# Optimization experiments

Measured on AMD Instinct MI355X. Metric: run time of the kernel, lower is better.

## Reference

```python
import jax, jax.numpy as jnp
import numpy as np

H = 512   # layer_size
D = 5     # dim
B = 64
T = 512
EPS = 1e-3  # Keras BatchNormalization default epsilon


def _p(key, shape, scale=0.05):
    return jax.random.normal(key, shape, dtype=jnp.float32) * scale


def setup_inputs() -> dict:
    key = jax.random.key(0)
    ks = jax.random.split(key, 32)
    inp = {
        "x": jax.random.normal(ks[0], (B, T, D), dtype=jnp.float32),
        # LSTM 1 (input D)
        "W1": _p(ks[1], (D, 4 * H)), "U1": _p(ks[2], (H, 4 * H)), "b1": jnp.zeros((4 * H,), jnp.float32),
        # BatchNorm on H features (inference: moving stats)
        "g1": jnp.ones((H,), jnp.float32), "be1": jnp.zeros((H,), jnp.float32),
        "m1": _p(ks[3], (H,), 0.1), "v1": jnp.ones((H,), jnp.float32) + jax.random.uniform(ks[4], (H,)) * 0.1,
        # LSTM 2 (input H)
        "W2": _p(ks[5], (H, 4 * H)), "U2": _p(ks[6], (H, 4 * H)), "b2": jnp.zeros((4 * H,), jnp.float32),
        # LSTM 3 (input H, returns last state only)
        "W3": _p(ks[7], (H, 4 * H)), "U3": _p(ks[8], (H, 4 * H)), "b3": jnp.zeros((4 * H,), jnp.float32),
        # dense head y
        "d1w": _p(ks[9], (H, 32)), "d1b": jnp.zeros((32,), jnp.float32),
        "g2": jnp.ones((32,), jnp.float32), "be2": jnp.zeros((32,), jnp.float32),
        "m2": _p(ks[10], (32,), 0.1), "v2": jnp.ones((32,), jnp.float32) + jax.random.uniform(ks[11], (32,)) * 0.1,
        "d2w": _p(ks[12], (32, 16)), "d2b": jnp.zeros((16,), jnp.float32),
        "hw": _p(ks[13], (16, 1)), "hb": jnp.zeros((1,), jnp.float32),
        # dense head z
        "d4w": _p(ks[14], (H, 128)), "d4b": jnp.zeros((128,), jnp.float32),
        "d5w": _p(ks[15], (128, 64)), "d5b": jnp.zeros((64,), jnp.float32),
        "rw": _p(ks[16], (64, D)), "rb": jnp.zeros((D,), jnp.float32),
    }
    return inp


def lstm(x, W, U, b):
    """Keras LSTM, gate order i,f,c,o. x: [B,T,din] -> (seq [B,T,H], h_T, c_T)."""
    xz = jnp.einsum('btd,dk->btk', x, W) + b  # precompute input projections [B,T,4H]

    def step(carry, xz_t):
        h, c = carry
        z = xz_t + h @ U
        i, f, g, o = jnp.split(z, 4, axis=-1)
        i = jax.nn.sigmoid(i)
        f = jax.nn.sigmoid(f)
        g = jnp.tanh(g)
        o = jax.nn.sigmoid(o)
        c = f * c + i * g
        h = o * jnp.tanh(c)
        return (h, c), h

    b_ = x.shape[0]
    h0 = jnp.zeros((b_, U.shape[0]), x.dtype)
    (hT, cT), hs = jax.lax.scan(step, (h0, h0), jnp.swapaxes(xz, 0, 1))
    return jnp.swapaxes(hs, 0, 1), hT, cT


def bn_inf(x, g, b, m, v):
    return (x - m) * (g / jnp.sqrt(v + EPS)) + b


def reference(x, W1, U1, b1, g1, be1, m1, v1, W2, U2, b2, W3, U3, b3,
              d1w, d1b, g2, be2, m2, v2, d2w, d2b, hw, hb,
              d4w, d4b, d5w, d5b, rw, rb):
    # inference: GaussianNoise / Dropout are identity
    x1, h1, s1 = lstm(x, W1, U1, b1)          # [B,T,H]
    xr = bn_inf(x1, g1, be1, m1, v1)
    x2, h2, s2 = lstm(xr, W2, U2, b2)         # [B,T,H]
    xs = x1 + x2                               # residual Add
    _, h3, s3 = lstm(xs, W3, U3, b3)           # last hidden state [B,H]
    xlast = h3
    # head y
    y = xlast @ d1w + d1b
    y = bn_inf(y, g2, be2, m2, v2)
    y = y @ d2w + d2b
    y = jax.nn.sigmoid(y @ hw + hb)            # [B,1]
    # head z
    z = xlast @ d4w + d4b
    z = z @ d5w + d5b
    z = z @ rw + rb                            # [B,D]
    return (y, z)
```

## Files before the change

### kernel.cpp

```cpp
#include <hip/hip_runtime.h>
#include <hip/hip_bf16.h>

typedef short bf16x8 __attribute__((ext_vector_type(8)));
typedef float f32x4 __attribute__((ext_vector_type(4)));
typedef unsigned short u16;
typedef unsigned int u32;
typedef unsigned long long u64;

#define EPSBN 1e-3f

__device__ __forceinline__ u16 f2b(float f){
  unsigned u = __float_as_uint(f);
  return (u16)((u + 0x7fffu + ((u >> 16) & 1u)) >> 16);
}
__device__ __forceinline__ float b2f(u16 v){ return __uint_as_float(((unsigned)v) << 16); }
__device__ __forceinline__ float sigm(float x){ return 1.f/(1.f + __expf(-x)); }
__device__ __forceinline__ float tanhx(float x){ return 2.f/(1.f + __expf(-2.f*x)) - 1.f; }

union U64x2 { u64 q[2]; bf16x8 v; };


__global__ void prep_sv(const float* __restrict__ g1, const float* __restrict__ be1,
                        const float* __restrict__ m1, const float* __restrict__ v1,
                        float* __restrict__ s, float* __restrict__ tv){
  int k = blockIdx.x*256 + threadIdx.x;
  if (k < 512){
    float sv = g1[k] * rsqrtf(v1[k] + EPSBN);
    s[k] = sv;
    tv[k] = be1[k] - m1[k]*sv;
  }
}

__global__ void prep_b2p(const float* __restrict__ W2, const float* __restrict__ b2,
                         const float* __restrict__ tv, float* __restrict__ out){
  int col = blockIdx.x*256 + threadIdx.x;
  float acc = b2[col];
  for (int k=0;k<512;++k) acc += tv[k] * W2[(size_t)k*2048 + col];
  out[col] = acc;
}

__global__ void transpose_pack(const float* __restrict__ in, const float* __restrict__ scale,
                               u16* __restrict__ out){
  __shared__ float tile[64][65];
  int k0 = blockIdx.x * 64;
  int c0 = blockIdx.y * 64;
  int t = threadIdx.x;
  int cc = t & 63, kk0 = (t >> 6) * 16;
  #pragma unroll
  for (int i=0;i<16;++i){
    float v = in[(size_t)(k0 + kk0 + i)*2048 + c0 + cc];
    if (scale) v *= scale[k0 + kk0 + i];
    tile[kk0 + i][cc] = v;
  }
  __syncthreads();
  int cc2 = t >> 2, kp = t & 3;
  int col = c0 + cc2;
  int hcol = col & 511;
  int row = (hcol >> 5)*128 + (col >> 9)*32 + ((hcol >> 4) & 1)*16 + (col & 15);
  bf16x8 v0, v1;
  #pragma unroll
  for (int i=0;i<8;++i){
    v0[i] = (short)f2b(tile[kp*16 + i][cc2]);
    v1[i] = (short)f2b(tile[kp*16 + 8 + i][cc2]);
  }
  u16* dst = out + (size_t)row*512 + k0 + kp*16;
  *(bf16x8*)dst = v0;
  *(bf16x8*)(dst + 8) = v1;
}

__global__ void pack_w1(const float* __restrict__ W1, u16* __restrict__ out){
  int r = blockIdx.x*256 + threadIdx.x;
  int wg = r >> 7, q = (r >> 5) & 3, jt = (r >> 4) & 1, jj = r & 15;
  int col = q*512 + wg*32 + jt*16 + jj;
  #pragma unroll
  for (int k=0;k<32;++k)
    out[(size_t)r*32 + k] = (k < 5) ? f2b(W1[(size_t)k*2048 + col]) : (u16)0;
}

__global__ void pack_x(const float* __restrict__ x, u16* __restrict__ out){
  int i = blockIdx.x*256 + threadIdx.x;
  int k = i & 31;
  int bt = i >> 5;
  out[i] = (k < 5) ? f2b(x[(size_t)bt*5 + k]) : (u16)0;
}

__device__ __forceinline__ void pollge(const u32* p, u32 target){
  while (__hip_atomic_load(p, __ATOMIC_RELAXED, __HIP_MEMORY_SCOPE_AGENT) < target) {}
}

__global__ void __launch_bounds__(512, 2) scan_all(
    const u16* __restrict__ Ure1, const u16* __restrict__ Ure2, const u16* __restrict__ Ure3,
    const u16* __restrict__ W1p,  const u16* __restrict__ W2p,  const u16* __restrict__ W3p,
    const u16* __restrict__ xpad,
    const float* __restrict__ b1, const float* __restrict__ b2p, const float* __restrict__ b3,
    u32* __restrict__ hbuf_all,
    u32* __restrict__ x1seq,
    u32* __restrict__ xsseq,
    float* __restrict__ h3out, u32* __restrict__ cnt)
{
  const int bid = blockIdx.x;
  const int phase = bid >> 6;
  const int b6 = bid & 63;
  const int g = b6 & 3, wg = b6 >> 2;
  const int tid = threadIdx.x;
  const int w = tid >> 6, l = tid & 63;
  const int lm = l & 15, lh = (l >> 4) & 3;
  const int kp = w & 3, jt = w >> 2;
  const int bg0 = g * 16;
  const int jp = tid & 15, gb = (tid >> 4) & 15;
  const int jt2 = jp >> 3;

  const u16* Ure  = phase == 0 ? Ure1 : (phase == 1 ? Ure2 : Ure3);
  const u16* Wre  = phase == 0 ? W1p  : (phase == 1 ? W2p  : W3p);
  const float* bias = phase == 0 ? b1 : (phase == 1 ? b2p : b3);
  u32* hbuf32 = hbuf_all + (size_t)phase * 32768;
  u32* seqout = phase == 0 ? x1seq : (phase == 1 ? xsseq : nullptr);
  const u32* upseq = phase == 1 ? x1seq : (phase == 2 ? xsseq : nullptr);

  u32* cq  = cnt + (phase*4 + g)*64;
  const u32* upq = (phase > 0) ? cnt + ((phase-1)*4 + g)*64 : nullptr;

  bf16x8 aU[4][4];
  #pragma unroll
  for (int q=0;q<4;++q){
    const u16* up = Ure + (size_t)(wg*128 + q*32 + jt*16 + lm)*512 + kp*128 + lh*8;
    #pragma unroll
    for (int ks=0;ks<4;++ks) aU[q][ks] = *(const bf16x8*)(up + ks*32);
  }
  bf16x8 aW[4][4];
  bf16x8 aW1[4];
  if (phase == 0){
    if (kp == 0){
      #pragma unroll
      for (int q=0;q<4;++q)
        aW1[q] = *(const bf16x8*)(Wre + (size_t)(wg*128 + q*32 + jt*16 + lm)*32 + lh*8);
    }
  } else {
    #pragma unroll
    for (int q=0;q<4;++q){
      const u16* wp = Wre + (size_t)(wg*128 + q*32 + jt*16 + lm)*512 + kp*128 + lh*8;
      #pragma unroll
      for (int ks=0;ks<4;++ks) aW[q][ks] = *(const bf16x8*)(wp + ks*32);
    }
  }

  float bias0[4], bias1[4];
  if (tid < 256){
    #pragma unroll
    for (int q=0;q<4;++q){
      bias0[q] = bias[q*512 + wg*32 + 2*jp];
      bias1[q] = bias[q*512 + wg*32 + 2*jp + 1];
    }
  }

  float cs0 = 0.f, cs1 = 0.f;

  __shared__ float zex[8][4][16][18];
  const u64* hbase = (const u64*)hbuf32;

  for (int t=0; t<512; ++t){
    f32x4 acc[4] = {};
    u32 rv = 0;

    if (phase == 0){
      if (kp == 0){
        bf16x8 bx = *(const bf16x8*)(xpad + ((size_t)(bg0+lm)*512 + t)*32 + lh*8);
        #pragma unroll
        for (int q=0;q<4;++q)
          acc[q] = __builtin_amdgcn_mfma_f32_16x16x32_bf16(aW1[q], bx, acc[q], 0,0,0);
      }
    } else {
      pollge(upq, (u32)(16*(t+1)));
      if (phase == 1 && tid < 256)
        rv = __hip_atomic_load(upseq + ((size_t)(bg0+gb)*512 + t)*256 + wg*16 + jp,
                               __ATOMIC_RELAXED, __HIP_MEMORY_SCOPE_AGENT);
      const u64* xp = (const u64*)upseq + ((size_t)(bg0+lm)*512 + t)*128 + kp*32 + lh*2;
      U64x2 xq[4];
      #pragma unroll
      for (int ks=0;ks<4;++ks){
        xq[ks].q[0] = __hip_atomic_load(xp + ks*8,     __ATOMIC_RELAXED, __HIP_MEMORY_SCOPE_AGENT);
        xq[ks].q[1] = __hip_atomic_load(xp + ks*8 + 1, __ATOMIC_RELAXED, __HIP_MEMORY_SCOPE_AGENT);
      }
      #pragma unroll
      for (int ks=0;ks<4;++ks){
        #pragma unroll
        for (int q=0;q<4;++q)
          acc[q] = __builtin_amdgcn_mfma_f32_16x16x32_bf16(aW[q][ks], xq[ks].v, acc[q], 0,0,0);
      }
    }

    pollge(cq, (u32)(16*t));
    {
      const u64* hp = hbase + (size_t)(((t+1)&1)*64 + bg0 + lm)*128 + kp*32 + lh*2;
      U64x2 hq[4];
      #pragma unroll
      for (int ks=0;ks<4;++ks){
        hq[ks].q[0] = __hip_atomic_load(hp + ks*8,     __ATOMIC_RELAXED, __HIP_MEMORY_SCOPE_AGENT);
        hq[ks].q[1] = __hip_atomic_load(hp + ks*8 + 1, __ATOMIC_RELAXED, __HIP_MEMORY_SCOPE_AGENT);
      }
      #pragma unroll
      for (int ks=0;ks<4;++ks){
        #pragma unroll
        for (int q=0;q<4;++q)
          acc[q] = __builtin_amdgcn_mfma_f32_16x16x32_bf16(aU[q][ks], hq[ks].v, acc[q], 0,0,0);
      }
    }

    #pragma unroll
    for (int q=0;q<4;++q){
      #pragma unroll
      for (int r=0;r<4;++r)
        zex[q*2+jt][kp][lh*4 + r][lm] = acc[q][r];
    }
    __syncthreads();

    if (tid < 256){
      const int r0 = (2*jp) & 15, r1 = r0 + 1;
      float zv0[4], zv1[4];
      #pragma unroll
      for (int q=0;q<4;++q){
        const int ti = q*2 + jt2;
        zv0[q] = zex[ti][0][r0][gb] + zex[ti][1][r0][gb]
               + zex[ti][2][r0][gb] + zex[ti][3][r0][gb] + bias0[q];
        zv1[q] = zex[ti][0][r1][gb] + zex[ti][1][r1][gb]
               + zex[ti][2][r1][gb] + zex[ti][3][r1][gb] + bias1[q];
      }
      float iv = sigm(zv0[0]), fv = sigm(zv0[1]), gv = tanhx(zv0[2]), ov = sigm(zv0[3]);
      cs0 = fv * cs0 + iv * gv;
      float hv0 = ov * tanhx(cs0);
      iv = sigm(zv1[0]); fv = sigm(zv1[1]); gv = tanhx(zv1[2]); ov = sigm(zv1[3]);
      cs1 = fv * cs1 + iv * gv;
      float hv1 = ov * tanhx(cs1);

      const u32 pw = (u32)f2b(hv0) | ((u32)f2b(hv1) << 16);
      __hip_atomic_store(hbuf32 + (size_t)((t&1)*64 + bg0 + gb)*256 + wg*16 + jp, pw,
                         __ATOMIC_RELAXED, __HIP_MEMORY_SCOPE_AGENT);
      if (phase == 0){
        __hip_atomic_store(seqout + ((size_t)(bg0+gb)*512 + t)*256 + wg*16 + jp, pw,
                           __ATOMIC_RELAXED, __HIP_MEMORY_SCOPE_AGENT);
      } else if (phase == 1){
        float x1r0 = b2f((u16)(rv & 0xffffu));
        float x1r1 = b2f((u16)(rv >> 16));
        u32 sv = (u32)f2b(x1r0 + hv0) | ((u32)f2b(x1r1 + hv1) << 16);
        __hip_atomic_store(seqout + ((size_t)(bg0+gb)*512 + t)*256 + wg*16 + jp, sv,
                           __ATOMIC_RELAXED, __HIP_MEMORY_SCOPE_AGENT);
      } else if (t == 511){
        h3out[(size_t)(bg0+gb)*512 + wg*32 + 2*jp]     = hv0;
        h3out[(size_t)(bg0+gb)*512 + wg*32 + 2*jp + 1] = hv1;
      }
    }
    __syncthreads();
    if (tid == 0)
      __hip_atomic_fetch_add(cq, 1u, __ATOMIC_RELAXED, __HIP_MEMORY_SCOPE_AGENT);
  }
}

__global__ void __launch_bounds__(256) head_k(
    const float* __restrict__ h3,
    const float* __restrict__ d1w, const float* __restrict__ d1b,
    const float* __restrict__ g2, const float* __restrict__ be2,
    const float* __restrict__ m2, const float* __restrict__ v2,
    const float* __restrict__ d2w, const float* __restrict__ d2b,
    const float* __restrict__ hw, const float* __restrict__ hb,
    const float* __restrict__ d4w, const float* __restrict__ d4b,
    const float* __restrict__ d5w, const float* __restrict__ d5b,
    const float* __restrict__ rw, const float* __restrict__ rb,
    float* __restrict__ out)
{
  __shared__ float hl[512];
  __shared__ float a1[32], a2[16], c1[128], c2[64];
  int b = blockIdx.x, t = threadIdx.x;
  for (int i=t; i<512; i+=256) hl[i] = h3[(size_t)b*512 + i];
  __syncthreads();
  if (t < 32){
    float acc = d1b[t];
    for (int k=0;k<512;++k) acc += hl[k] * d1w[(size_t)k*32 + t];
    a1[t] = (acc - m2[t]) * (g2[t] * rsqrtf(v2[t] + EPSBN)) + be2[t];
  } else if (t >= 128){
    int i = t - 128;
    float acc = d4b[i];
    for (int k=0;k<512;++k) acc += hl[k] * d4w[(size_t)k*128 + i];
    c1[i] = acc;
  }
  __syncthreads();
  if (t < 16){
    float acc = d2b[t];
    for (int k=0;k<32;++k) acc += a1[k] * d2w[k*16 + t];
    a2[t] = acc;
  } else if (t >= 64 && t < 128){
    int i = t - 64;
    float acc = d5b[i];
    for (int k=0;k<128;++k) acc += c1[k] * d5w[k*64 + i];
    c2[i] = acc;
  }
  __syncthreads();
  if (t == 0){
    float acc = hb[0];
    for (int k=0;k<16;++k) acc += a2[k] * hw[k];
    out[b] = 1.f/(1.f + __expf(-acc));
  } else if (t >= 32 && t < 37){
    int i = t - 32;
    float acc = rb[i];
    for (int k=0;k<64;++k) acc += c2[k] * rw[k*5 + i];
    out[64 + b*5 + i] = acc;
  }
}

extern "C" void kernel_launch(void* const* d_in, const int* in_sizes, int n_in,
                              void* d_out, int out_size, void* d_ws, size_t ws_size,
                              hipStream_t stream)
{
  const float* x   = (const float*)d_in[0];
  const float* W1  = (const float*)d_in[1];
  const float* U1  = (const float*)d_in[2];
  const float* b1  = (const float*)d_in[3];
  const float* g1  = (const float*)d_in[4];
  const float* be1 = (const float*)d_in[5];
  const float* m1  = (const float*)d_in[6];
  const float* v1  = (const float*)d_in[7];
  const float* W2  = (const float*)d_in[8];
  const float* U2  = (const float*)d_in[9];
  const float* b2  = (const float*)d_in[10];
  const float* W3  = (const float*)d_in[11];
  const float* U3  = (const float*)d_in[12];
  const float* b3  = (const float*)d_in[13];
  const float* d1w = (const float*)d_in[14];
  const float* d1b = (const float*)d_in[15];
  const float* g2  = (const float*)d_in[16];
  const float* be2 = (const float*)d_in[17];
  const float* m2  = (const float*)d_in[18];
  const float* v2  = (const float*)d_in[19];
  const float* d2w = (const float*)d_in[20];
  const float* d2b = (const float*)d_in[21];
  const float* hw  = (const float*)d_in[22];
  const float* hb  = (const float*)d_in[23];
  const float* d4w = (const float*)d_in[24];
  const float* d4b = (const float*)d_in[25];
  const float* d5w = (const float*)d_in[26];
  const float* d5b = (const float*)d_in[27];
  const float* rw  = (const float*)d_in[28];
  const float* rb  = (const float*)d_in[29];

  char* ws = (char*)d_ws;
  constexpr size_t SZ_W   = 2048ull*512*2;
  constexpr size_t o_Ure1 = 0;
  constexpr size_t o_Ure2 = o_Ure1 + SZ_W;
  constexpr size_t o_Ure3 = o_Ure2 + SZ_W;
  constexpr size_t o_W2p  = o_Ure3 + SZ_W;
  constexpr size_t o_W3p  = o_W2p + SZ_W;
  constexpr size_t o_W1p  = o_W3p + SZ_W;
  constexpr size_t o_xpad = o_W1p + 2048ull*32*2;
  constexpr size_t o_b2p  = o_xpad + 64ull*512*32*2;
  constexpr size_t o_s    = o_b2p + 2048ull*4;
  constexpr size_t o_tv   = o_s + 512ull*4;
  constexpr size_t o_h3   = o_tv + 512ull*4;
  constexpr size_t o_h    = o_h3 + 64ull*512*4;
  constexpr size_t SZ_HP  = 2ull*64*256*4;
  constexpr size_t SZ_H   = 3*SZ_HP;
  constexpr size_t o_cnt  = o_h + SZ_H;
  constexpr size_t o_x1   = o_cnt + 4096;
  constexpr size_t o_xs   = o_x1 + 64ull*512*512*2;

  u16* Ure1 = (u16*)(ws + o_Ure1);
  u16* Ure2 = (u16*)(ws + o_Ure2);
  u16* Ure3 = (u16*)(ws + o_Ure3);
  u16* W2p  = (u16*)(ws + o_W2p);
  u16* W3p  = (u16*)(ws + o_W3p);
  u16* W1p  = (u16*)(ws + o_W1p);
  u16* xpad = (u16*)(ws + o_xpad);
  u32* x1p  = (u32*)(ws + o_x1);
  u32* xsp  = (u32*)(ws + o_xs);

  hipMemsetAsync(ws + o_h, 0, SZ_H + 4096, stream);

  prep_sv<<<dim3(2), dim3(256), 0, stream>>>(g1, be1, m1, v1, (float*)(ws+o_s), (float*)(ws+o_tv));
  transpose_pack<<<dim3(8,32), dim3(256), 0, stream>>>(U1, nullptr, Ure1);
  transpose_pack<<<dim3(8,32), dim3(256), 0, stream>>>(U2, nullptr, Ure2);
  transpose_pack<<<dim3(8,32), dim3(256), 0, stream>>>(U3, nullptr, Ure3);
  transpose_pack<<<dim3(8,32), dim3(256), 0, stream>>>(W3, nullptr, W3p);
  transpose_pack<<<dim3(8,32), dim3(256), 0, stream>>>(W2, (const float*)(ws+o_s), W2p);
  prep_b2p<<<dim3(8), dim3(256), 0, stream>>>(W2, b2, (const float*)(ws+o_tv), (float*)(ws+o_b2p));
  pack_w1<<<dim3(8), dim3(256), 0, stream>>>(W1, W1p);
  pack_x<<<dim3(4096), dim3(256), 0, stream>>>(x, xpad);

  scan_all<<<dim3(192), dim3(512), 0, stream>>>(
      Ure1, Ure2, Ure3, W1p, W2p, W3p, xpad,
      b1, (const float*)(ws+o_b2p), b3,
      (u32*)(ws+o_h), x1p, xsp,
      (float*)(ws+o_h3), (u32*)(ws+o_cnt));

  head_k<<<dim3(64), dim3(256), 0, stream>>>((const float*)(ws+o_h3),
      d1w, d1b, g2, be2, m2, v2, d2w, d2b, hw, hb, d4w, d4b, d5w, d5b, rw, rb,
      (float*)d_out);
}
```

Measured before the change: 2.629 ms.

## Prefetch next-step input projection and signal per-wave completion before barrier

Moves the next timestep's input loads (x, or the upstream layer's sequence plus residual) so they are issued after the current recurrent state is fetched, overlapping them with the U-matrix MFMAs. Each of the four writing waves now drains its own stores and bumps the counter itself, so completion is signalled before the trailing block barrier rather than after it. Polling targets are scaled by four to match the per-wave increments. Empty asm constraints pin the weight fragments in registers. The cost is higher register pressure, and the per-wave vmcnt(0) wait plus relaxed ordering depend on the stores being visible before the counter increment.

```diff
diff --git a/kernel.cpp b/kernel.cpp
--- a/kernel.cpp
+++ b/kernel.cpp
@@ -93,9 +93,7 @@
     const u16* __restrict__ W1p,  const u16* __restrict__ W2p,  const u16* __restrict__ W3p,
     const u16* __restrict__ xpad,
     const float* __restrict__ b1, const float* __restrict__ b2p, const float* __restrict__ b3,
-    u32* __restrict__ hbuf_all,
-    u32* __restrict__ x1seq,
-    u32* __restrict__ xsseq,
+    u32* __restrict__ hbuf_all, u32* __restrict__ x1seq, u32* __restrict__ xsseq,
     float* __restrict__ h3out, u32* __restrict__ cnt)
 {
   const int bid = blockIdx.x;
@@ -125,22 +123,30 @@
   for (int q=0;q<4;++q){
     const u16* up = Ure + (size_t)(wg*128 + q*32 + jt*16 + lm)*512 + kp*128 + lh*8;
     #pragma unroll
-    for (int ks=0;ks<4;++ks) aU[q][ks] = *(const bf16x8*)(up + ks*32);
+    for (int ks=0;ks<4;++ks){
+      aU[q][ks] = *(const bf16x8*)(up + ks*32);
+      asm volatile("" : "+v"(aU[q][ks]));
+    }
   }
   bf16x8 aW[4][4];
   bf16x8 aW1[4];
   if (phase == 0){
     if (kp == 0){
       #pragma unroll
-      for (int q=0;q<4;++q)
+      for (int q=0;q<4;++q){
         aW1[q] = *(const bf16x8*)(Wre + (size_t)(wg*128 + q*32 + jt*16 + lm)*32 + lh*8);
+        asm volatile("" : "+v"(aW1[q]));
+      }
     }
   } else {
     #pragma unroll
     for (int q=0;q<4;++q){
       const u16* wp = Wre + (size_t)(wg*128 + q*32 + jt*16 + lm)*512 + kp*128 + lh*8;
       #pragma unroll
-      for (int ks=0;ks<4;++ks) aW[q][ks] = *(const bf16x8*)(wp + ks*32);
+      for (int ks=0;ks<4;++ks){
+        aW[q][ks] = *(const bf16x8*)(wp + ks*32);
+        asm volatile("" : "+v"(aW[q][ks]));
+      }
     }
   }
 
@@ -158,29 +164,36 @@
   __shared__ float zex[8][4][16][18];
   const u64* hbase = (const u64*)hbuf32;
 
+  U64x2 xq[4];
+  bf16x8 bx;
+  u32 rv = 0;
+  if (phase == 0){
+    if (kp == 0)
+      bx = *(const bf16x8*)(xpad + ((size_t)(bg0+lm)*512 + 0)*32 + lh*8);
+  } else {
+    pollge(upq, 64u);
+    const u64* xp = (const u64*)upseq + ((size_t)(bg0+lm)*512 + 0)*128 + kp*32 + lh*2;
+    #pragma unroll
+    for (int ks=0;ks<4;++ks){
+      xq[ks].q[0] = __hip_atomic_load(xp + ks*8,     __ATOMIC_RELAXED, __HIP_MEMORY_SCOPE_AGENT);
+      xq[ks].q[1] = __hip_atomic_load(xp + ks*8 + 1, __ATOMIC_RELAXED, __HIP_MEMORY_SCOPE_AGENT);
+    }
+    if (phase == 1 && tid < 256)
+      rv = __hip_atomic_load(upseq + ((size_t)(bg0+gb)*512 + 0)*256 + wg*16 + jp,
+                             __ATOMIC_RELAXED, __HIP_MEMORY_SCOPE_AGENT);
+  }
+
   for (int t=0; t<512; ++t){
     f32x4 acc[4] = {};
-    u32 rv = 0;
+    const u32 rvc = rv;
 
     if (phase == 0){
       if (kp == 0){
-        bf16x8 bx = *(const bf16x8*)(xpad + ((size_t)(bg0+lm)*512 + t)*32 + lh*8);
         #pragma unroll
         for (int q=0;q<4;++q)
           acc[q] = __builtin_amdgcn_mfma_f32_16x16x32_bf16(aW1[q], bx, acc[q], 0,0,0);
       }
     } else {
-      pollge(upq, (u32)(16*(t+1)));
-      if (phase == 1 && tid < 256)
-        rv = __hip_atomic_load(upseq + ((size_t)(bg0+gb)*512 + t)*256 + wg*16 + jp,
-                               __ATOMIC_RELAXED, __HIP_MEMORY_SCOPE_AGENT);
-      const u64* xp = (const u64*)upseq + ((size_t)(bg0+lm)*512 + t)*128 + kp*32 + lh*2;
-      U64x2 xq[4];
-      #pragma unroll
-      for (int ks=0;ks<4;++ks){
-        xq[ks].q[0] = __hip_atomic_load(xp + ks*8,     __ATOMIC_RELAXED, __HIP_MEMORY_SCOPE_AGENT);
-        xq[ks].q[1] = __hip_atomic_load(xp + ks*8 + 1, __ATOMIC_RELAXED, __HIP_MEMORY_SCOPE_AGENT);
-      }
       #pragma unroll
       for (int ks=0;ks<4;++ks){
         #pragma unroll
@@ -189,21 +202,40 @@
       }
     }
 
-    pollge(cq, (u32)(16*t));
+    pollge(cq, 64u*(u32)t);
+    U64x2 hq[4];
     {
       const u64* hp = hbase + (size_t)(((t+1)&1)*64 + bg0 + lm)*128 + kp*32 + lh*2;
-      U64x2 hq[4];
       #pragma unroll
       for (int ks=0;ks<4;++ks){
         hq[ks].q[0] = __hip_atomic_load(hp + ks*8,     __ATOMIC_RELAXED, __HIP_MEMORY_SCOPE_AGENT);
         hq[ks].q[1] = __hip_atomic_load(hp + ks*8 + 1, __ATOMIC_RELAXED, __HIP_MEMORY_SCOPE_AGENT);
       }
-      #pragma unroll
-      for (int ks=0;ks<4;++ks){
+    }
+
+    if (t < 511){
+      if (phase == 0){
+        if (kp == 0)
+          bx = *(const bf16x8*)(xpad + ((size_t)(bg0+lm)*512 + (t+1))*32 + lh*8);
+      } else {
+        pollge(upq, 64u*(u32)(t+2));
+        const u64* xp = (const u64*)upseq + ((size_t)(bg0+lm)*512 + (t+1))*128 + kp*32 + lh*2;
         #pragma unroll
-        for (int q=0;q<4;++q)
-          acc[q] = __builtin_amdgcn_mfma_f32_16x16x32_bf16(aU[q][ks], hq[ks].v, acc[q], 0,0,0);
-      }
+        for (int ks=0;ks<4;++ks){
+          xq[ks].q[0] = __hip_atomic_load(xp + ks*8,     __ATOMIC_RELAXED, __HIP_MEMORY_SCOPE_AGENT);
+          xq[ks].q[1] = __hip_atomic_load(xp + ks*8 + 1, __ATOMIC_RELAXED, __HIP_MEMORY_SCOPE_AGENT);
+        }
+        if (phase == 1 && tid < 256)
+          rv = __hip_atomic_load(upseq + ((size_t)(bg0+gb)*512 + (t+1))*256 + wg*16 + jp,
+                                 __ATOMIC_RELAXED, __HIP_MEMORY_SCOPE_AGENT);
+      }
+    }
+
+    #pragma unroll
+    for (int ks=0;ks<4;++ks){
+      #pragma unroll
+      for (int q=0;q<4;++q)
+        acc[q] = __builtin_amdgcn_mfma_f32_16x16x32_bf16(aU[q][ks], hq[ks].v, acc[q], 0,0,0);
     }
 
     #pragma unroll
@@ -239,8 +271,8 @@
         __hip_atomic_store(seqout + ((size_t)(bg0+gb)*512 + t)*256 + wg*16 + jp, pw,
                            __ATOMIC_RELAXED, __HIP_MEMORY_SCOPE_AGENT);
       } else if (phase == 1){
-        float x1r0 = b2f((u16)(rv & 0xffffu));
-        float x1r1 = b2f((u16)(rv >> 16));
+        float x1r0 = b2f((u16)(rvc & 0xffffu));
+        float x1r1 = b2f((u16)(rvc >> 16));
         u32 sv = (u32)f2b(x1r0 + hv0) | ((u32)f2b(x1r1 + hv1) << 16);
         __hip_atomic_store(seqout + ((size_t)(bg0+gb)*512 + t)*256 + wg*16 + jp, sv,
                            __ATOMIC_RELAXED, __HIP_MEMORY_SCOPE_AGENT);
@@ -248,10 +280,11 @@
         h3out[(size_t)(bg0+gb)*512 + wg*32 + 2*jp]     = hv0;
         h3out[(size_t)(bg0+gb)*512 + wg*32 + 2*jp + 1] = hv1;
       }
+      asm volatile("s_waitcnt vmcnt(0)" ::: "memory");
+      if ((tid & 63) == 0)
+        __hip_atomic_fetch_add(cq, 1u, __ATOMIC_RELAXED, __HIP_MEMORY_SCOPE_AGENT);
     }
     __syncthreads();
-    if (tid == 0)
-      __hip_atomic_fetch_add(cq, 1u, __ATOMIC_RELAXED, __HIP_MEMORY_SCOPE_AGENT);
   }
 }
 
```

Measured after the change: 3.475 ms. 32.2% more time.
